# Optimization experiments

Hardware: AMD Instinct MI355X
Metric: run time of the kernel (lower is better)

The kernel has to match this reference:

```python
import jax, jax.numpy as jnp
import numpy as np

VOCAB = 50000
D = 256
NUM_GROUPS = 2
NUM_BEAMS = 4
MAX_LEN = 24
DIV_STRENGTH = 0.5


def setup_inputs() -> dict:
    key = jax.random.key(0)
    k1, k2, k3, k4 = jax.random.split(key, 4)
    B, S = 8, 128
    src = jax.random.normal(k1, (B, S, D), jnp.float32)
    We = jax.random.normal(k2, (D, D), jnp.float32) * (1.0 / np.sqrt(D))
    Emb = jax.random.normal(k3, (VOCAB, D), jnp.float32) * 0.02
    Wout = jax.random.normal(k4, (D, VOCAB), jnp.float32) * (1.0 / np.sqrt(D))
    return {"src": src, "We": We, "Emb": Emb, "Wout": Wout}


def _beam_search(src, We, Emb, Wout):
    B = src.shape[0]
    K, V, L = NUM_BEAMS, VOCAB, MAX_LEN

    # encoder: linear projection; decoder context = mean-pooled encoder output
    enc_out = jnp.einsum('bsd,de->bse', src, We)      # [B, S, D]
    ctx = enc_out.mean(axis=1)                        # [B, D]
    ctx_rep = jnp.repeat(ctx, K, axis=0)              # [B*K, D]
    beam_ids = jnp.arange(K)[:, None, None]           # [K,1,1]

    all_seqs, all_scores = [], []
    for g in range(NUM_GROUPS):
        prev = jnp.stack(all_seqs) if g > 0 else None  # [g, B, K, L]

        def step(carry, t, prev=prev):
            seqs, gs = carry                           # [B,K,L] int32, [B,K] f32
            tok = jax.lax.dynamic_index_in_dim(seqs, t - 1, axis=2, keepdims=False)  # [B,K]
            h = Emb[tok.reshape(-1)] + ctx_rep         # [B*K, D]
            logits = h @ Wout                          # [B*K, V]
            scores = jax.nn.log_softmax(logits, axis=-1).reshape(B, K, V)
            if prev is not None:
                # diversity penalty: subtract strength once per token present
                # anywhere (any batch, pos < t) in prev group's beam b (unique() semantics)
                posmask = (jnp.arange(L) < t).astype(scores.dtype)   # [L]
                w = jnp.broadcast_to(posmask, (K, B, L))

                def presence(pseq):                    # pseq: [B,K,L]
                    tok_t = pseq.transpose(1, 0, 2)    # [K,B,L]
                    cnt = jnp.zeros((K, V), scores.dtype).at[beam_ids, tok_t].add(w)
                    return (cnt > 0).astype(scores.dtype)

                pen = jax.vmap(presence)(prev).sum(axis=0)           # [K,V]
                scores = scores - DIV_STRENGTH * pen[None, :, :]
            total = (gs[:, :, None] + scores).reshape(B, K * V)
            topk_scores, topk_idx = jax.lax.top_k(total, K)          # [B,K]
            beam_idx = topk_idx // V
            next_tok = topk_idx % V
            seqs = jnp.take_along_axis(seqs, beam_idx[:, :, None], axis=1)
            seqs = seqs.at[:, :, t].set(next_tok)
            return (seqs, topk_scores), None

        init_scores = jnp.full((B, K), -1e9, jnp.float32).at[:, 0].set(0.0)
        init_seqs = jnp.zeros((B, K, L), jnp.int32).at[:, :, 0].set(1)  # BOS=1
        (seqs, gscores), _ = jax.lax.scan(step, (init_seqs, init_scores), jnp.arange(1, L))
        all_seqs.append(seqs)
        all_scores.append(gscores)

    return jnp.concatenate(all_seqs, axis=1), jnp.concatenate(all_scores, axis=1)


def reference(src, We, Emb, Wout):
    # returns (final_sequences [B, G*K, L] int32, final_scores [B, G*K] f32)
    return _beam_search(src, We, Emb, Wout)
```

## Files before the change

kernel.cpp:

```cpp
#include <hip/hip_runtime.h>
#include <math.h>

#define VOCAB 50000
#define DM 256
#define NB 8
#define NK 4
#define SL 24
#define NROW 32
#define CBLK 256
#define NXB 196
#define NPART NXB
#define DIVS 0.5f
#define NCH 49
#define SCH 1024

__device__ __forceinline__ bool cbetter(float av, int ai, float bv, int bi) {
  return (av > bv) || (av == bv && ai < bi);
}

__device__ __forceinline__ void merge4(const float* av, const int* ai,
                                       const float* bv, const int* bi,
                                       float* rv, int* ri) {
  int x = 0, y = 0;
#pragma unroll
  for (int j = 0; j < 4; ++j) {
    bool ta = cbetter(av[x], ai[x], bv[y], bi[y]);
    rv[j] = ta ? av[x] : bv[y];
    ri[j] = ta ? ai[x] : bi[y];
    if (ta) ++x; else ++y;
  }
}

__global__ void k_prep(const float* __restrict__ src, const float* __restrict__ We,
                       float* __restrict__ ctx) {
  int b = blockIdx.x, d = threadIdx.x;
  __shared__ float sm[DM];
  const float* p = src + (size_t)b * 128 * DM + d;
  float s = 0.f;
  for (int i = 0; i < 128; ++i) s += p[i * DM];
  sm[d] = s * (1.f / 128.f);
  __syncthreads();
  float acc = 0.f;
  for (int dp = 0; dp < DM; ++dp) acc += sm[dp] * We[dp * DM + d];
  ctx[b * DM + d] = acc;
}

__global__ void k_eprep(const float* __restrict__ Emb, const float* __restrict__ ctx,
                        const int* __restrict__ seq, float* __restrict__ eg, int t) {
  int r = blockIdx.x, d = threadIdx.x;
  int tok = seq[r * SL + (t - 1)];
  eg[r * DM + d] = Emb[(size_t)tok * DM + d] + ctx[(r >> 2) * DM + d];
}

__global__ __launch_bounds__(512) void k_logits(
    const float* __restrict__ Wout, const float* __restrict__ eg,
    float* __restrict__ logits, float* __restrict__ pm, float* __restrict__ ps) {
  int tid = threadIdx.x;
  int lane = tid & 63, wq = tid >> 6;
  int c0 = blockIdx.x * CBLK + lane * 4;
  bool valid = (c0 + 3 < VOCAB);
  const float* wbase = Wout + (valid ? c0 : (VOCAB - 4));
  int rb = __builtin_amdgcn_readfirstlane(wq) * 4;
  const float* e0 = eg + (size_t)rb * DM;
  float acc[4][4];
#pragma unroll
  for (int r = 0; r < 4; ++r)
#pragma unroll
    for (int c = 0; c < 4; ++c) acc[r][c] = 0.f;

  for (int d = 0; d < DM; d += 8) {
    float4 w[8];
#pragma unroll
    for (int j = 0; j < 8; ++j)
      w[j] = *reinterpret_cast<const float4*>(wbase + (size_t)(d + j) * VOCAB);
#pragma unroll
    for (int r = 0; r < 4; ++r) {
      const float* ep = e0 + r * DM + d;
      const float4 ea = *reinterpret_cast<const float4*>(ep);
      const float4 eb = *reinterpret_cast<const float4*>(ep + 4);
#pragma unroll
      for (int c = 0; c < 4; ++c) {
        float a = acc[r][c];
        a = fmaf(ea.x, (&w[0].x)[c], a);
        a = fmaf(ea.y, (&w[1].x)[c], a);
        a = fmaf(ea.z, (&w[2].x)[c], a);
        a = fmaf(ea.w, (&w[3].x)[c], a);
        a = fmaf(eb.x, (&w[4].x)[c], a);
        a = fmaf(eb.y, (&w[5].x)[c], a);
        a = fmaf(eb.z, (&w[6].x)[c], a);
        a = fmaf(eb.w, (&w[7].x)[c], a);
        acc[r][c] = a;
      }
    }
  }
  if (valid) {
#pragma unroll
    for (int r = 0; r < 4; ++r) {
      float4 o = make_float4(acc[r][0], acc[r][1], acc[r][2], acc[r][3]);
      *reinterpret_cast<float4*>(&logits[(size_t)(rb + r) * VOCAB + c0]) = o;
    }
  }
#pragma unroll
  for (int r = 0; r < 4; ++r) {
    float m = valid ? fmaxf(fmaxf(acc[r][0], acc[r][1]), fmaxf(acc[r][2], acc[r][3]))
                    : -INFINITY;
#pragma unroll
    for (int o = 32; o >= 1; o >>= 1) m = fmaxf(m, __shfl_xor(m, o));
    float sv = 0.f;
    if (valid && m != -INFINITY) {
      sv = expf(acc[r][0] - m) + expf(acc[r][1] - m) +
           expf(acc[r][2] - m) + expf(acc[r][3] - m);
    }
#pragma unroll
    for (int o = 32; o >= 1; o >>= 1) sv += __shfl_xor(sv, o);
    if (lane == 0) {
      pm[(size_t)(rb + r) * NPART + blockIdx.x] = m;
      ps[(size_t)(rb + r) * NPART + blockIdx.x] = sv;
    }
  }
}

__global__ __launch_bounds__(256) void k_topk_s1(
    const float* __restrict__ logits, const float* __restrict__ pm,
    const float* __restrict__ ps, const float* __restrict__ gs_src,
    const int* __restrict__ minpos, float* __restrict__ s1v,
    int* __restrict__ s1i, int t, int g) {
  int b = blockIdx.x / NCH, c = blockIdx.x % NCH, tid = threadIdx.x;
  int lane = tid & 63, wave = tid >> 6;
  __shared__ float gsv[NK], lsev[NK];
  __shared__ float lv[256][4];
  __shared__ int li[256][4];
  if (tid < NK) gsv[tid] = gs_src[b * NK + tid];
  {
    int row = b * NK + wave;
    const float* pmr = pm + (size_t)row * NPART;
    const float* psr = ps + (size_t)row * NPART;
    float M = -INFINITY, S = 0.f;
    for (int j = lane; j < NPART; j += 64) {
      float mj = pmr[j];
      if (mj != -INFINITY) {
        float sj = psr[j];
        float Mn = fmaxf(M, mj);
        S = (M == -INFINITY) ? sj * expf(mj - Mn)
                             : S * expf(M - Mn) + sj * expf(mj - Mn);
        M = Mn;
      }
    }
#pragma unroll
    for (int o = 32; o >= 1; o >>= 1) {
      float Mo = __shfl_xor(M, o);
      float So = __shfl_xor(S, o);
      if (Mo != -INFINITY) {
        float Mn = fmaxf(M, Mo);
        S = (M == -INFINITY) ? So * expf(Mo - Mn)
                             : S * expf(M - Mn) + So * expf(Mo - Mn);
        M = Mn;
      }
    }
    if (lane == 0) lsev[wave] = M + logf(S);
  }
  __syncthreads();

  float tv[4]; int ti[4];
#pragma unroll
  for (int j = 0; j < 4; ++j) { tv[j] = -INFINITY; ti[j] = 0x7fffffff; }

  int v = c * SCH + tid * 4;
  for (int k = 0; k < NK; ++k) {
    float gsk = gsv[k], lsek = lsev[k];
    const float* lrow = logits + (size_t)(b * NK + k) * VOCAB;
    const int* mp = minpos + (size_t)k * VOCAB;
    if (v + 3 < VOCAB) {
      float4 x4 = *reinterpret_cast<const float4*>(lrow + v);
      float xs[4] = {x4.x, x4.y, x4.z, x4.w};
      int pen[4] = {0, 0, 0, 0};
      if (g) {
        int4 m4 = *reinterpret_cast<const int4*>(mp + v);
        pen[0] = m4.x < t; pen[1] = m4.y < t; pen[2] = m4.z < t; pen[3] = m4.w < t;
      }
#pragma unroll
      for (int i = 0; i < 4; ++i) {
        float sc = xs[i] - lsek;
        if (pen[i]) sc -= DIVS;
        float x = gsk + sc;
        int idx = k * VOCAB + v + i;
        if (cbetter(x, idx, tv[3], ti[3])) {
          int pos = 3;
          if (cbetter(x, idx, tv[2], ti[2])) { tv[3]=tv[2]; ti[3]=ti[2]; pos=2;
            if (cbetter(x, idx, tv[1], ti[1])) { tv[2]=tv[1]; ti[2]=ti[1]; pos=1;
              if (cbetter(x, idx, tv[0], ti[0])) { tv[1]=tv[0]; ti[1]=ti[0]; pos=0; } } }
          tv[pos] = x; ti[pos] = idx;
        }
      }
    } else {
#pragma unroll
      for (int i = 0; i < 4; ++i) {
        int vv = v + i;
        if (vv >= VOCAB) break;
        float sc = lrow[vv] - lsek;
        if (g && mp[vv] < t) sc -= DIVS;
        float x = gsk + sc;
        int idx = k * VOCAB + vv;
        if (cbetter(x, idx, tv[3], ti[3])) {
          int pos = 3;
          if (cbetter(x, idx, tv[2], ti[2])) { tv[3]=tv[2]; ti[3]=ti[2]; pos=2;
            if (cbetter(x, idx, tv[1], ti[1])) { tv[2]=tv[1]; ti[2]=ti[1]; pos=1;
              if (cbetter(x, idx, tv[0], ti[0])) { tv[1]=tv[0]; ti[1]=ti[0]; pos=0; } } }
          tv[pos] = x; ti[pos] = idx;
        }
      }
    }
  }
#pragma unroll
  for (int j = 0; j < 4; ++j) { lv[tid][j] = tv[j]; li[tid][j] = ti[j]; }
  __syncthreads();
  for (int s = 128; s >= 1; s >>= 1) {
    if (tid < s) {
      float av[4], bv[4], rv[4]; int ai[4], bi[4], ri[4];
#pragma unroll
      for (int j = 0; j < 4; ++j) { av[j]=lv[tid][j]; ai[j]=li[tid][j]; bv[j]=lv[tid+s][j]; bi[j]=li[tid+s][j]; }
      merge4(av, ai, bv, bi, rv, ri);
#pragma unroll
      for (int j = 0; j < 4; ++j) { lv[tid][j]=rv[j]; li[tid][j]=ri[j]; }
    }
    __syncthreads();
  }
  if (tid == 0) {
#pragma unroll
    for (int j = 0; j < 4; ++j) {
      s1v[(b * NCH + c) * 4 + j] = lv[0][j];
      s1i[(b * NCH + c) * 4 + j] = li[0][j];
    }
  }
}

__global__ __launch_bounds__(128) void k_topk_s2(
    const float* __restrict__ s1v, const int* __restrict__ s1i,
    const int* __restrict__ seq_src, float* __restrict__ gs_dst,
    int* __restrict__ seq_dst, int t, int g, float* __restrict__ out) {
  int b = blockIdx.x, tid = threadIdx.x;
  __shared__ float lv[64][4];
  __shared__ int li[64][4];
  __shared__ int oldseq[NK * SL];
  __shared__ float selv[NK];
  __shared__ int selb[NK], selt[NK];
  if (tid < 64) {
#pragma unroll
    for (int j = 0; j < 4; ++j) {
      if (tid < NCH) { lv[tid][j] = s1v[(b * NCH + tid) * 4 + j]; li[tid][j] = s1i[(b * NCH + tid) * 4 + j]; }
      else { lv[tid][j] = -INFINITY; li[tid][j] = 0x7fffffff; }
    }
  }
  if (tid < NK * SL) oldseq[tid] = seq_src[b * NK * SL + tid];
  __syncthreads();
  for (int s = 32; s >= 1; s >>= 1) {
    if (tid < s) {
      float av[4], bv[4], rv[4]; int ai[4], bi[4], ri[4];
#pragma unroll
      for (int j = 0; j < 4; ++j) { av[j]=lv[tid][j]; ai[j]=li[tid][j]; bv[j]=lv[tid+s][j]; bi[j]=li[tid+s][j]; }
      merge4(av, ai, bv, bi, rv, ri);
#pragma unroll
      for (int j = 0; j < 4; ++j) { lv[tid][j]=rv[j]; li[tid][j]=ri[j]; }
    }
    __syncthreads();
  }
  if (tid == 0) {
#pragma unroll
    for (int j = 0; j < 4; ++j) {
      selv[j] = lv[0][j];
      selb[j] = li[0][j] / VOCAB;
      selt[j] = li[0][j] % VOCAB;
    }
  }
  __syncthreads();
  if (tid < NK * SL) {
    int j = tid / SL, l = tid % SL;
    int tok = (l == t) ? selt[j] : oldseq[selb[j] * SL + l];
    seq_dst[b * NK * SL + tid] = tok;
    if (t == SL - 1) out[(size_t)b * (2 * NK * SL) + (g * NK + j) * SL + l] = (float)tok;
  }
  if (tid < NK) {
    gs_dst[b * NK + tid] = selv[tid];
    if (t == SL - 1) out[NB * 2 * NK * SL + b * (2 * NK) + g * NK + tid] = selv[tid];
  }
}

__global__ void k_init(int* __restrict__ seqA, float* __restrict__ gsA) {
  int i = threadIdx.x;
  seqA[i] = (i % SL == 0) ? 1 : 0;
  if (i < NB * NK) gsA[i] = ((i & 3) == 0) ? 0.f : -1e9f;
}

__global__ void k_minpos_init(int* __restrict__ minpos) {
  int i = blockIdx.x * 256 + threadIdx.x;
  if (i < NK * VOCAB) minpos[i] = 1 << 30;
}

__global__ void k_minpos_scatter(const int* __restrict__ seq, int* __restrict__ minpos) {
  int i = threadIdx.x;
  int l = i % SL;
  int k = (i / SL) % NK;
  int tok = seq[i];
  atomicMin(&minpos[(size_t)k * VOCAB + tok], l);
}

extern "C" void kernel_launch(void* const* d_in, const int* in_sizes, int n_in,
                              void* d_out, int out_size, void* d_ws, size_t ws_size,
                              hipStream_t stream) {
  (void)in_sizes; (void)n_in; (void)out_size; (void)ws_size;
  const float* src  = (const float*)d_in[0];
  const float* We   = (const float*)d_in[1];
  const float* Emb  = (const float*)d_in[2];
  const float* Wout = (const float*)d_in[3];
  float* out = (float*)d_out;
  char* ws = (char*)d_ws;
  size_t off = 0;
  auto carve = [&](size_t bytes) {
    char* p = ws + off;
    off += (bytes + 255) & ~(size_t)255;
    return p;
  };
  float* ctx    = (float*)carve((size_t)NB * DM * 4);
  float* eg     = (float*)carve((size_t)NROW * DM * 4);
  float* logits = (float*)carve((size_t)NROW * VOCAB * 4);
  float* pm     = (float*)carve((size_t)NROW * NPART * 4);
  float* ps     = (float*)carve((size_t)NROW * NPART * 4);
  int*   seqA   = (int*)carve((size_t)NB * NK * SL * 4);
  int*   seqB   = (int*)carve((size_t)NB * NK * SL * 4);
  float* gsA    = (float*)carve((size_t)NROW * 4);
  float* gsB    = (float*)carve((size_t)NROW * 4);
  int*   minpos = (int*)carve((size_t)NK * VOCAB * 4);
  float* s1v    = (float*)carve((size_t)NB * NCH * 4 * 4);
  int*   s1i    = (int*)carve((size_t)NB * NCH * 4 * 4);

  hipLaunchKernelGGL(k_prep, dim3(NB), dim3(DM), 0, stream, src, We, ctx);

  for (int g = 0; g < 2; ++g) {
    hipLaunchKernelGGL(k_init, dim3(1), dim3(768), 0, stream, seqA, gsA);
    for (int t = 1; t < SL; ++t) {
      int* ssrc = ((t - 1) & 1) ? seqB : seqA;
      int* sdst = (t & 1) ? seqB : seqA;
      float* gsrc = ((t - 1) & 1) ? gsB : gsA;
      float* gdst = (t & 1) ? gsB : gsA;
      hipLaunchKernelGGL(k_eprep, dim3(NROW), dim3(DM), 0, stream,
                         Emb, ctx, ssrc, eg, t);
      hipLaunchKernelGGL(k_logits, dim3(NXB), dim3(512), 0, stream,
                         Wout, eg, logits, pm, ps);
      hipLaunchKernelGGL(k_topk_s1, dim3(NB * NCH), dim3(256), 0, stream,
                         logits, pm, ps, gsrc, minpos, s1v, s1i, t, g);
      hipLaunchKernelGGL(k_topk_s2, dim3(NB), dim3(128), 0, stream,
                         s1v, s1i, ssrc, gdst, sdst, t, g, out);
    }
    if (g == 0) {
      hipLaunchKernelGGL(k_minpos_init, dim3((NK * VOCAB + 255) / 256), dim3(256), 0, stream, minpos);
      hipLaunchKernelGGL(k_minpos_scatter, dim3(1), dim3(768), 0, stream, seqB, minpos);
    }
  }
}
```

Measured before the change: 2.349 ms.

## Fuse per-block top-4 candidate selection into logits kernel and drop logits buffer

```diff
diff --git a/kernel.cpp b/kernel.cpp
--- a/kernel.cpp
+++ b/kernel.cpp
@@ -10,9 +10,9 @@
 #define CBLK 256
 #define NXB 196
 #define NPART NXB
+#define NCAND (NXB*4)
 #define DIVS 0.5f
-#define NCH 49
-#define SCH 1024
+#define CINV 0x7fffffff
 
 __device__ __forceinline__ bool cbetter(float av, int ai, float bv, int bi) {
   return (av > bv) || (av == bv && ai < bi);
@@ -54,7 +54,8 @@
 
 __global__ __launch_bounds__(512) void k_logits(
     const float* __restrict__ Wout, const float* __restrict__ eg,
-    float* __restrict__ logits, float* __restrict__ pm, float* __restrict__ ps) {
+    const int* __restrict__ minpos, float* __restrict__ pm, float* __restrict__ ps,
+    float* __restrict__ ckey, int* __restrict__ cvp, int t, int g) {
   int tid = threadIdx.x;
   int lane = tid & 63, wq = tid >> 6;
   int c0 = blockIdx.x * CBLK + lane * 4;
@@ -93,15 +94,9 @@
       }
     }
   }
-  if (valid) {
-#pragma unroll
-    for (int r = 0; r < 4; ++r) {
-      float4 o = make_float4(acc[r][0], acc[r][1], acc[r][2], acc[r][3]);
-      *reinterpret_cast<float4*>(&logits[(size_t)(rb + r) * VOCAB + c0]) = o;
-    }
-  }
 #pragma unroll
   for (int r = 0; r < 4; ++r) {
+    int row = rb + r;
     float m = valid ? fmaxf(fmaxf(acc[r][0], acc[r][1]), fmaxf(acc[r][2], acc[r][3]))
                     : -INFINITY;
 #pragma unroll
@@ -114,23 +109,75 @@
 #pragma unroll
     for (int o = 32; o >= 1; o >>= 1) sv += __shfl_xor(sv, o);
     if (lane == 0) {
-      pm[(size_t)(rb + r) * NPART + blockIdx.x] = m;
-      ps[(size_t)(rb + r) * NPART + blockIdx.x] = sv;
-    }
-  }
-}
-
-__global__ __launch_bounds__(256) void k_topk_s1(
-    const float* __restrict__ logits, const float* __restrict__ pm,
-    const float* __restrict__ ps, const float* __restrict__ gs_src,
-    const int* __restrict__ minpos, float* __restrict__ s1v,
-    int* __restrict__ s1i, int t, int g) {
-  int b = blockIdx.x / NCH, c = blockIdx.x % NCH, tid = threadIdx.x;
+      pm[(size_t)row * NPART + blockIdx.x] = m;
+      ps[(size_t)row * NPART + blockIdx.x] = sv;
+    }
+    int kk = row & 3;
+    int pen[4] = {0, 0, 0, 0};
+    if (g && valid) {
+      int4 m4 = *reinterpret_cast<const int4*>(minpos + (size_t)kk * VOCAB + c0);
+      pen[0] = m4.x < t; pen[1] = m4.y < t; pen[2] = m4.z < t; pen[3] = m4.w < t;
+    }
+    float kv[4]; int vp[4];
+#pragma unroll
+    for (int j = 0; j < 4; ++j) { kv[j] = -INFINITY; vp[j] = CINV; }
+#pragma unroll
+    for (int c = 0; c < 4; ++c) {
+      float key = valid ? (acc[r][c] - (pen[c] ? 0.5f : 0.0f)) : -INFINITY;
+      int v_ = valid ? ((c0 + c) | (pen[c] << 16)) : CINV;
+      int cc = v_ & 0xFFFF;
+      if (cbetter(key, cc, kv[3], vp[3] & 0xFFFF)) {
+        int pos = 3;
+        if (cbetter(key, cc, kv[2], vp[2] & 0xFFFF)) { kv[3]=kv[2]; vp[3]=vp[2]; pos=2;
+          if (cbetter(key, cc, kv[1], vp[1] & 0xFFFF)) { kv[2]=kv[1]; vp[2]=vp[1]; pos=1;
+            if (cbetter(key, cc, kv[0], vp[0] & 0xFFFF)) { kv[1]=kv[0]; vp[1]=vp[0]; pos=0; } } }
+        kv[pos] = key; vp[pos] = v_;
+      }
+    }
+#pragma unroll
+    for (int off = 32; off >= 1; off >>= 1) {
+      float ov[4]; int op[4];
+#pragma unroll
+      for (int j = 0; j < 4; ++j) { ov[j] = __shfl_xor(kv[j], off); op[j] = __shfl_xor(vp[j], off); }
+      float rv[4]; int rp[4];
+      int x = 0, y = 0;
+#pragma unroll
+      for (int j = 0; j < 4; ++j) {
+        bool ta = cbetter(kv[x], vp[x] & 0xFFFF, ov[y], op[y] & 0xFFFF);
+        rv[j] = ta ? kv[x] : ov[y];
+        rp[j] = ta ? vp[x] : op[y];
+        if (ta) ++x; else ++y;
+      }
+#pragma unroll
+      for (int j = 0; j < 4; ++j) { kv[j] = rv[j]; vp[j] = rp[j]; }
+    }
+    if (lane == 0) {
+#pragma unroll
+      for (int j = 0; j < 4; ++j) {
+        ckey[(size_t)row * NCAND + blockIdx.x * 4 + j] = kv[j];
+        cvp[(size_t)row * NCAND + blockIdx.x * 4 + j] = vp[j];
+      }
+    }
+  }
+}
+
+__global__ __launch_bounds__(256) void k_sel(
+    const float* __restrict__ ckey, const int* __restrict__ cvp,
+    const float* __restrict__ pm, const float* __restrict__ ps,
+    const float* __restrict__ gs_src, const int* __restrict__ seq_src,
+    const float* __restrict__ Emb, const float* __restrict__ ctx,
+    float* __restrict__ gs_dst, int* __restrict__ seq_dst,
+    float* __restrict__ eg, int t, int g, float* __restrict__ out) {
+  int b = blockIdx.x, tid = threadIdx.x;
   int lane = tid & 63, wave = tid >> 6;
   __shared__ float gsv[NK], lsev[NK];
   __shared__ float lv[256][4];
   __shared__ int li[256][4];
+  __shared__ int oldseq[NK * SL];
+  __shared__ float selv[NK];
+  __shared__ int selb[NK], selt[NK];
   if (tid < NK) gsv[tid] = gs_src[b * NK + tid];
+  if (tid < NK * SL) oldseq[tid] = seq_src[b * NK * SL + tid];
   {
     int row = b * NK + wave;
     const float* pmr = pm + (size_t)row * NPART;
@@ -163,97 +210,31 @@
 
   float tv[4]; int ti[4];
 #pragma unroll
-  for (int j = 0; j < 4; ++j) { tv[j] = -INFINITY; ti[j] = 0x7fffffff; }
-
-  int v = c * SCH + tid * 4;
-  for (int k = 0; k < NK; ++k) {
-    float gsk = gsv[k], lsek = lsev[k];
-    const float* lrow = logits + (size_t)(b * NK + k) * VOCAB;
-    const int* mp = minpos + (size_t)k * VOCAB;
-    if (v + 3 < VOCAB) {
-      float4 x4 = *reinterpret_cast<const float4*>(lrow + v);
-      float xs[4] = {x4.x, x4.y, x4.z, x4.w};
-      int pen[4] = {0, 0, 0, 0};
-      if (g) {
-        int4 m4 = *reinterpret_cast<const int4*>(mp + v);
-        pen[0] = m4.x < t; pen[1] = m4.y < t; pen[2] = m4.z < t; pen[3] = m4.w < t;
-      }
-#pragma unroll
-      for (int i = 0; i < 4; ++i) {
-        float sc = xs[i] - lsek;
-        if (pen[i]) sc -= DIVS;
-        float x = gsk + sc;
-        int idx = k * VOCAB + v + i;
-        if (cbetter(x, idx, tv[3], ti[3])) {
-          int pos = 3;
-          if (cbetter(x, idx, tv[2], ti[2])) { tv[3]=tv[2]; ti[3]=ti[2]; pos=2;
-            if (cbetter(x, idx, tv[1], ti[1])) { tv[2]=tv[1]; ti[2]=ti[1]; pos=1;
-              if (cbetter(x, idx, tv[0], ti[0])) { tv[1]=tv[0]; ti[1]=ti[0]; pos=0; } } }
-          tv[pos] = x; ti[pos] = idx;
-        }
-      }
-    } else {
-#pragma unroll
-      for (int i = 0; i < 4; ++i) {
-        int vv = v + i;
-        if (vv >= VOCAB) break;
-        float sc = lrow[vv] - lsek;
-        if (g && mp[vv] < t) sc -= DIVS;
-        float x = gsk + sc;
-        int idx = k * VOCAB + vv;
-        if (cbetter(x, idx, tv[3], ti[3])) {
-          int pos = 3;
-          if (cbetter(x, idx, tv[2], ti[2])) { tv[3]=tv[2]; ti[3]=ti[2]; pos=2;
-            if (cbetter(x, idx, tv[1], ti[1])) { tv[2]=tv[1]; ti[2]=ti[1]; pos=1;
-              if (cbetter(x, idx, tv[0], ti[0])) { tv[1]=tv[0]; ti[1]=ti[0]; pos=0; } } }
-          tv[pos] = x; ti[pos] = idx;
-        }
-      }
+  for (int j = 0; j < 4; ++j) { tv[j] = -INFINITY; ti[j] = CINV; }
+  for (int c = tid; c < NK * NCAND; c += 256) {
+    int r = c / NCAND, e = c - r * NCAND;
+    float key = ckey[(size_t)(b * NK + r) * NCAND + e];
+    int vp = cvp[(size_t)(b * NK + r) * NCAND + e];
+    if (vp == CINV) continue;
+    int pen = (vp >> 16) & 1;
+    int col = vp & 0xFFFF;
+    float l = key + (pen ? 0.5f : 0.0f);
+    float sc = l - lsev[r];
+    if (pen) sc -= DIVS;
+    float x = gsv[r] + sc;
+    int idx = r * VOCAB + col;
+    if (cbetter(x, idx, tv[3], ti[3])) {
+      int pos = 3;
+      if (cbetter(x, idx, tv[2], ti[2])) { tv[3]=tv[2]; ti[3]=ti[2]; pos=2;
+        if (cbetter(x, idx, tv[1], ti[1])) { tv[2]=tv[1]; ti[2]=ti[1]; pos=1;
+          if (cbetter(x, idx, tv[0], ti[0])) { tv[1]=tv[0]; ti[1]=ti[0]; pos=0; } } }
+      tv[pos] = x; ti[pos] = idx;
     }
   }
 #pragma unroll
   for (int j = 0; j < 4; ++j) { lv[tid][j] = tv[j]; li[tid][j] = ti[j]; }
   __syncthreads();
   for (int s = 128; s >= 1; s >>= 1) {
-    if (tid < s) {
-      float av[4], bv[4], rv[4]; int ai[4], bi[4], ri[4];
-#pragma unroll
-      for (int j = 0; j < 4; ++j) { av[j]=lv[tid][j]; ai[j]=li[tid][j]; bv[j]=lv[tid+s][j]; bi[j]=li[tid+s][j]; }
-      merge4(av, ai, bv, bi, rv, ri);
-#pragma unroll
-      for (int j = 0; j < 4; ++j) { lv[tid][j]=rv[j]; li[tid][j]=ri[j]; }
-    }
-    __syncthreads();
-  }
-  if (tid == 0) {
-#pragma unroll
-    for (int j = 0; j < 4; ++j) {
-      s1v[(b * NCH + c) * 4 + j] = lv[0][j];
-      s1i[(b * NCH + c) * 4 + j] = li[0][j];
-    }
-  }
-}
-
-__global__ __launch_bounds__(128) void k_topk_s2(
-    const float* __restrict__ s1v, const int* __restrict__ s1i,
-    const int* __restrict__ seq_src, float* __restrict__ gs_dst,
-    int* __restrict__ seq_dst, int t, int g, float* __restrict__ out) {
-  int b = blockIdx.x, tid = threadIdx.x;
-  __shared__ float lv[64][4];
-  __shared__ int li[64][4];
-  __shared__ int oldseq[NK * SL];
-  __shared__ float selv[NK];
-  __shared__ int selb[NK], selt[NK];
-  if (tid < 64) {
-#pragma unroll
-    for (int j = 0; j < 4; ++j) {
-      if (tid < NCH) { lv[tid][j] = s1v[(b * NCH + tid) * 4 + j]; li[tid][j] = s1i[(b * NCH + tid) * 4 + j]; }
-      else { lv[tid][j] = -INFINITY; li[tid][j] = 0x7fffffff; }
-    }
-  }
-  if (tid < NK * SL) oldseq[tid] = seq_src[b * NK * SL + tid];
-  __syncthreads();
-  for (int s = 32; s >= 1; s >>= 1) {
     if (tid < s) {
       float av[4], bv[4], rv[4]; int ai[4], bi[4], ri[4];
 #pragma unroll
@@ -282,6 +263,14 @@
   if (tid < NK) {
     gs_dst[b * NK + tid] = selv[tid];
     if (t == SL - 1) out[NB * 2 * NK * SL + b * (2 * NK) + g * NK + tid] = selv[tid];
+  }
+  if (t < SL - 1) {
+    int d = tid;
+#pragma unroll
+    for (int j = 0; j < NK; ++j) {
+      int nt_ = selt[j];
+      eg[(size_t)(b * NK + j) * DM + d] = Emb[(size_t)nt_ * DM + d] + ctx[b * DM + d];
+    }
   }
 }
 
@@ -322,16 +311,15 @@
   };
   float* ctx    = (float*)carve((size_t)NB * DM * 4);
   float* eg     = (float*)carve((size_t)NROW * DM * 4);
-  float* logits = (float*)carve((size_t)NROW * VOCAB * 4);
   float* pm     = (float*)carve((size_t)NROW * NPART * 4);
   float* ps     = (float*)carve((size_t)NROW * NPART * 4);
+  float* ckey   = (float*)carve((size_t)NROW * NCAND * 4);
+  int*   cvp    = (int*)carve((size_t)NROW * NCAND * 4);
   int*   seqA   = (int*)carve((size_t)NB * NK * SL * 4);
   int*   seqB   = (int*)carve((size_t)NB * NK * SL * 4);
   float* gsA    = (float*)carve((size_t)NROW * 4);
   float* gsB    = (float*)carve((size_t)NROW * 4);
   int*   minpos = (int*)carve((size_t)NK * VOCAB * 4);
-  float* s1v    = (float*)carve((size_t)NB * NCH * 4 * 4);
-  int*   s1i    = (int*)carve((size_t)NB * NCH * 4 * 4);
 
   hipLaunchKernelGGL(k_prep, dim3(NB), dim3(DM), 0, stream, src, We, ctx);
 
@@ -342,14 +330,14 @@
       int* sdst = (t & 1) ? seqB : seqA;
       float* gsrc = ((t - 1) & 1) ? gsB : gsA;
       float* gdst = (t & 1) ? gsB : gsA;
-      hipLaunchKernelGGL(k_eprep, dim3(NROW), dim3(DM), 0, stream,
-                         Emb, ctx, ssrc, eg, t);
+      if (t == 1)
+        hipLaunchKernelGGL(k_eprep, dim3(NROW), dim3(DM), 0, stream,
+                           Emb, ctx, ssrc, eg, t);
       hipLaunchKernelGGL(k_logits, dim3(NXB), dim3(512), 0, stream,
-                         Wout, eg, logits, pm, ps);
-      hipLaunchKernelGGL(k_topk_s1, dim3(NB * NCH), dim3(256), 0, stream,
-                         logits, pm, ps, gsrc, minpos, s1v, s1i, t, g);
-      hipLaunchKernelGGL(k_topk_s2, dim3(NB), dim3(128), 0, stream,
-                         s1v, s1i, ssrc, gdst, sdst, t, g, out);
+                         Wout, eg, minpos, pm, ps, ckey, cvp, t, g);
+      hipLaunchKernelGGL(k_sel, dim3(NB), dim3(256), 0, stream,
+                         ckey, cvp, pm, ps, gsrc, ssrc, Emb, ctx,
+                         gdst, sdst, eg, t, g, out);
     }
     if (g == 0) {
       hipLaunchKernelGGL(k_minpos_init, dim3((NK * VOCAB + 255) / 256), dim3(256), 0, stream, minpos);
```

Result: slower. 4.791 ms (+104.0%).
